# Performance work log

Hardware: AMD Instinct MI355X
Metric: run time of the kernel (lower is better)

Reference implementation:

```python
import jax, jax.numpy as jnp
import numpy as np

N_NODES = 50000
N_EDGES = 800000
D_IN = 256
D_HID = 256
D_OUT = 128


def setup_inputs() -> dict:
    key = jax.random.key(0)
    ks = jax.random.split(key, 6)
    z = jax.random.normal(ks[0], (N_NODES, D_IN), dtype=jnp.float32)
    edge_index = jax.random.randint(ks[1], (2, N_EDGES), 0, N_NODES, dtype=jnp.int32)
    W1 = jax.random.normal(ks[2], (D_IN, D_HID), dtype=jnp.float32) / np.sqrt(D_IN).astype(np.float32)
    b1 = jnp.zeros((D_HID,), dtype=jnp.float32)
    W2 = jax.random.normal(ks[3], (D_HID, D_OUT), dtype=jnp.float32) / np.sqrt(D_HID).astype(np.float32)
    b2 = jnp.zeros((D_OUT,), dtype=jnp.float32)
    return {"z": z, "edge_index": edge_index, "W1": W1, "b1": b1, "W2": W2, "b2": b2}


def _gcn_conv(x, W, b, src, dst, n_nodes):
    """GCNConv: x' = D^{-1/2} (A + I) D^{-1/2} (x W) + b (symmetric norm, self-loops)."""
    x = x @ W  # [n, d_out] dense transform first (as in PyG GCNConv)
    loop = jnp.arange(n_nodes, dtype=src.dtype)
    s = jnp.concatenate([src, loop])  # add self-loops
    d = jnp.concatenate([dst, loop])
    deg = jax.ops.segment_sum(jnp.ones(s.shape, dtype=x.dtype), d, num_segments=n_nodes)
    dinv = jnp.where(deg > 0, jax.lax.rsqrt(deg), 0.0)
    norm = dinv[s] * dinv[d]  # per-edge symmetric normalization
    msgs = x[s] * norm[:, None]  # gather + scale
    out = jax.ops.segment_sum(msgs, d, num_segments=n_nodes)  # scatter-add
    return out + b


def reference(z, edge_index, W1, b1, W2, b2):
    src, dst = edge_index[0], edge_index[1]
    n = z.shape[0]
    h = jax.nn.relu(_gcn_conv(z, W1, b1, src, dst, n))
    return _gcn_conv(h, W2, b2, src, dst, n)
```

## Files before the change

### kernel.cpp

```cpp
#include <hip/hip_runtime.h>


#define N_NODES 50000
#define N_EDGES 800000
#define D_IN    256
#define D_HID   256
#define D_OUT   128

typedef unsigned int uint32;
typedef unsigned short u16;

typedef __attribute__((ext_vector_type(8))) short bf16x8;
typedef __attribute__((ext_vector_type(4))) float f32x4;

__device__ __forceinline__ u16 f2bf_rne(float f) {
    union { float f; uint32 u; } c; c.f = f;
    uint32 u = c.u;
    u += 0x7FFFu + ((u >> 16) & 1u);
    return (u16)(u >> 16);
}
__device__ __forceinline__ float bf_lo(uint32 p) {
    union { uint32 u; float f; } c; c.u = p << 16; return c.f;
}
__device__ __forceinline__ float bf_hi(uint32 p) {
    union { uint32 u; float f; } c; c.u = p & 0xFFFF0000u; return c.f;
}


__global__ __launch_bounds__(256) void prep_kernel(const float* __restrict__ z,
                                                   const int* __restrict__ dst,
                                                   const float* __restrict__ W1,
                                                   const float* __restrict__ W2,
                                                   u16* __restrict__ zb,
                                                   u16* __restrict__ w1t,
                                                   u16* __restrict__ w2t,
                                                   int* __restrict__ cnt,
                                                   int* __restrict__ rank) {
    const int g = blockIdx.x * 256 + threadIdx.x;
    const int GT = gridDim.x * 256;

    for (int c = g; c < N_NODES * D_IN / 8; c += GT) {
        int i = c * 8;
        float4 a = *(const float4*)(z + i);
        float4 d = *(const float4*)(z + i + 4);
        uint4 pk;
        pk.x = (uint32)f2bf_rne(a.x) | ((uint32)f2bf_rne(a.y) << 16);
        pk.y = (uint32)f2bf_rne(a.z) | ((uint32)f2bf_rne(a.w) << 16);
        pk.z = (uint32)f2bf_rne(d.x) | ((uint32)f2bf_rne(d.y) << 16);
        pk.w = (uint32)f2bf_rne(d.z) | ((uint32)f2bf_rne(d.w) << 16);
        *(uint4*)(zb + i) = pk;
    }
    for (int idx = g; idx < D_IN * D_HID + D_HID * D_OUT; idx += GT) {
        if (idx < D_IN * D_HID) {
            int nrow = idx >> 8, kcol = idx & 255;
            w1t[idx] = f2bf_rne(W1[kcol * D_HID + nrow]);
        } else {
            int j = idx - D_IN * D_HID;
            int nrow = j >> 8, kcol = j & 255;
            w2t[j] = f2bf_rne(W2[kcol * D_OUT + nrow]);
        }
    }
    for (int i = g; i < N_EDGES; i += GT)
        rank[i] = atomicAdd(&cnt[dst[i]], 1);
}


__global__ __launch_bounds__(1024) void scan_kernel(const int* __restrict__ cnt,
                                                    float* __restrict__ dinv,
                                                    int* __restrict__ row_ptr, int n) {
    __shared__ int wtot[16];
    __shared__ int carry_s;
    const int t = threadIdx.x;
    const int lane = t & 63, w = t >> 6;
    if (t == 0) carry_s = 0;
    __syncthreads();

    const int n4 = n >> 2;
    for (int base = 0; base < n4; base += 1024) {
        int i4 = base + t;
        int4 v = make_int4(0, 0, 0, 0);
        if (i4 < n4) v = ((const int4*)cnt)[i4];
        int s = v.x + v.y + v.z + v.w;
        int x = s;
        #pragma unroll
        for (int off = 1; off < 64; off <<= 1) {
            int u = __shfl_up(x, off, 64);
            if (lane >= off) x += u;
        }
        if (lane == 63) wtot[w] = x;
        __syncthreads();

        int wbase = 0;
        #pragma unroll
        for (int j = 0; j < 16; ++j) if (j < w) wbase += wtot[j];
        int excl = carry_s + wbase + x - s;
        if (i4 < n4) {
            int4 rp;
            rp.x = excl;
            rp.y = rp.x + v.x;
            rp.z = rp.y + v.y;
            rp.w = rp.z + v.z;
            ((int4*)row_ptr)[i4] = rp;
            float4 dv;
            dv.x = rsqrtf((float)(v.x + 1));
            dv.y = rsqrtf((float)(v.y + 1));
            dv.z = rsqrtf((float)(v.z + 1));
            dv.w = rsqrtf((float)(v.w + 1));
            ((float4*)dinv)[i4] = dv;
        }
        __syncthreads();
        if (t == 0) {
            int tot = 0;
            #pragma unroll
            for (int j = 0; j < 16; ++j) tot += wtot[j];
            carry_s += tot;
        }
        __syncthreads();
    }
    if (t == 0) row_ptr[n] = carry_s;
}


__global__ void fill_kernel(const int* __restrict__ src, const int* __restrict__ dst,
                            const int* __restrict__ rank, const int* __restrict__ row_ptr,
                            int* __restrict__ col, int n_edges) {
    int i = blockIdx.x * blockDim.x + threadIdx.x;
    if (i < n_edges)
        col[row_ptr[dst[i]] + rank[i]] = src[i];
}


template <int NT>
__global__ __launch_bounds__(256, 4) void gemm_bf16_kernel(const u16* __restrict__ A,
                                                           const u16* __restrict__ BT,
                                                           u16* __restrict__ C, int M) {
    const int K = 256;
    __shared__ short As[128 * 32];
    __shared__ short Bs[128 * 32];

    const int m0 = blockIdx.x * 128;
    const int n0 = blockIdx.y * 128;
    const int t  = threadIdx.x;
    const int w  = t >> 6;
    const int lane = t & 63;
    const int lm = lane & 15;
    const int lq = lane >> 4;
    const int wm = w & 1;
    const int wn = w >> 1;

    f32x4 acc[4][4] = {};

    for (int k0 = 0; k0 < K; k0 += 32) {
        #pragma unroll
        for (int j = 0; j < 2; ++j) {
            int c = w * 128 + j * 64 + lane;
            int row = c >> 2;
            int kc = k0 + (c & 3) * 8;
            int gm = m0 + row; if (gm >= M) gm = M - 1;
            const u16* gpa = A  + (size_t)gm * K + kc;
            const u16* gpb = BT + (size_t)(n0 + row) * K + kc;
            __builtin_amdgcn_global_load_lds(
                (const __attribute__((address_space(1))) void*)gpa,
                (__attribute__((address_space(3))) void*)(As + (w * 128 + j * 64) * 8),
                16, 0, 0);
            __builtin_amdgcn_global_load_lds(
                (const __attribute__((address_space(1))) void*)gpb,
                (__attribute__((address_space(3))) void*)(Bs + (w * 128 + j * 64) * 8),
                16, 0, 0);
        }
        __syncthreads();

        bf16x8 af[4], bf[4];
        #pragma unroll
        for (int mt = 0; mt < 4; ++mt)
            af[mt] = *(const bf16x8*)&As[(wm * 64 + mt * 16 + lm) * 32 + lq * 8];
        #pragma unroll
        for (int nt = 0; nt < 4; ++nt)
            bf[nt] = *(const bf16x8*)&Bs[(wn * 64 + nt * 16 + lm) * 32 + lq * 8];

        #pragma unroll
        for (int mt = 0; mt < 4; ++mt)
            #pragma unroll
            for (int nt = 0; nt < 4; ++nt)
                acc[mt][nt] = __builtin_amdgcn_mfma_f32_16x16x32_bf16(
                    af[mt], bf[nt], acc[mt][nt], 0, 0, 0);

        __syncthreads();
    }

    #pragma unroll
    for (int mt = 0; mt < 4; ++mt) {
        #pragma unroll
        for (int r = 0; r < 4; ++r) {
            int gm = m0 + wm * 64 + mt * 16 + lq * 4 + r;
            if (gm < M) {
                #pragma unroll
                for (int nt = 0; nt < 4; ++nt) {
                    int gn = n0 + wn * 64 + nt * 16 + lm;
                    C[(size_t)gm * NT + gn] = f2bf_rne(acc[mt][nt][r]);
                }
            }
        }
    }
}


template <int D, bool RELU, bool OUTBF>
__global__ __launch_bounds__(256) void aggregate_kernel(const u16* __restrict__ x,
                                                        const int* __restrict__ row_ptr,
                                                        const int* __restrict__ col,
                                                        const float* __restrict__ dinv,
                                                        const float* __restrict__ bias,
                                                        void* __restrict__ outp, int n_nodes) {
    constexpr int VPL = D / 64;
    int node = (blockIdx.x * blockDim.x + threadIdx.x) >> 6;
    int lane = threadIdx.x & 63;
    if (node >= n_nodes) return;
    const int c0 = lane * VPL;

    float di = dinv[node];
    float acc[4][VPL] = {};

    {
        float w = di * di;
        const u16* xs = x + (size_t)node * D + c0;
        if constexpr (VPL == 4) {
            uint2 p = *(const uint2*)xs;
            acc[0][0] = bf_lo(p.x) * w;
            acc[0][1] = bf_hi(p.x) * w;
            acc[0][2] = bf_lo(p.y) * w;
            acc[0][3] = bf_hi(p.y) * w;
        } else {
            uint32 p = *(const uint32*)xs;
            acc[0][0] = bf_lo(p) * w;
            acc[0][1] = bf_hi(p) * w;
        }
    }

    int e0 = row_ptr[node], e1 = row_ptr[node + 1];
    int e = e0;
    for (; e + 4 <= e1; e += 4) {
        #pragma unroll
        for (int u = 0; u < 4; ++u) {
            int s  = col[e + u];
            float w = dinv[s] * di;
            const u16* xs = x + (size_t)s * D + c0;
            if constexpr (VPL == 4) {
                uint2 p = *(const uint2*)xs;
                acc[u][0] = fmaf(bf_lo(p.x), w, acc[u][0]);
                acc[u][1] = fmaf(bf_hi(p.x), w, acc[u][1]);
                acc[u][2] = fmaf(bf_lo(p.y), w, acc[u][2]);
                acc[u][3] = fmaf(bf_hi(p.y), w, acc[u][3]);
            } else {
                uint32 p = *(const uint32*)xs;
                acc[u][0] = fmaf(bf_lo(p), w, acc[u][0]);
                acc[u][1] = fmaf(bf_hi(p), w, acc[u][1]);
            }
        }
    }
    for (; e < e1; ++e) {
        int s  = col[e];
        float w = dinv[s] * di;
        const u16* xs = x + (size_t)s * D + c0;
        if constexpr (VPL == 4) {
            uint2 p = *(const uint2*)xs;
            acc[0][0] = fmaf(bf_lo(p.x), w, acc[0][0]);
            acc[0][1] = fmaf(bf_hi(p.x), w, acc[0][1]);
            acc[0][2] = fmaf(bf_lo(p.y), w, acc[0][2]);
            acc[0][3] = fmaf(bf_hi(p.y), w, acc[0][3]);
        } else {
            uint32 p = *(const uint32*)xs;
            acc[0][0] = fmaf(bf_lo(p), w, acc[0][0]);
            acc[0][1] = fmaf(bf_hi(p), w, acc[0][1]);
        }
    }

    float v[VPL];
    #pragma unroll
    for (int j = 0; j < VPL; ++j) {
        float s = acc[0][j] + acc[1][j] + acc[2][j] + acc[3][j] + bias[c0 + j];
        v[j] = RELU ? fmaxf(s, 0.0f) : s;
    }

    if constexpr (OUTBF) {
        u16* op = (u16*)outp + (size_t)node * D + c0;
        if constexpr (VPL == 4) {
            uint2 pk;
            pk.x = (uint32)f2bf_rne(v[0]) | ((uint32)f2bf_rne(v[1]) << 16);
            pk.y = (uint32)f2bf_rne(v[2]) | ((uint32)f2bf_rne(v[3]) << 16);
            *(uint2*)op = pk;
        } else {
            *(uint32*)op = (uint32)f2bf_rne(v[0]) | ((uint32)f2bf_rne(v[1]) << 16);
        }
    } else {
        float* op = (float*)outp + (size_t)node * D + c0;
        #pragma unroll
        for (int j = 0; j < VPL; ++j) op[j] = v[j];
    }
}


extern "C" void kernel_launch(void* const* d_in, const int* in_sizes, int n_in,
                              void* d_out, int out_size, void* d_ws, size_t ws_size,
                              hipStream_t stream) {
    const float* z  = (const float*)d_in[0];
    const int*   ei = (const int*)d_in[1];
    const float* W1 = (const float*)d_in[2];
    const float* b1 = (const float*)d_in[3];
    const float* W2 = (const float*)d_in[4];
    const float* b2 = (const float*)d_in[5];
    float* out = (float*)d_out;

    const int Nn = N_NODES, E = N_EDGES;
    const int* srcp = ei;
    const int* dstp = ei + E;

    char* ws = (char*)d_ws;
    size_t off = 0;
    auto alloc = [&](size_t bytes) -> char* {
        char* p = ws + off;
        off += (bytes + 511) & ~(size_t)511;
        return p;
    };
    u16*   zb     = (u16*)  alloc((size_t)Nn * D_IN * 2);
    u16*   w1t    = (u16*)  alloc((size_t)D_IN * D_HID * 2);
    u16*   w2t    = (u16*)  alloc((size_t)D_HID * D_OUT * 2);
    u16*   x1b    = (u16*)  alloc((size_t)Nn * D_HID * 2);
    u16*   hb     = (u16*)  alloc((size_t)Nn * D_HID * 2);
    u16*   h2b    = (u16*)  alloc((size_t)Nn * D_OUT * 2);
    int*   cnt    = (int*)  alloc((size_t)Nn * 4);
    float* dinv   = (float*)alloc((size_t)Nn * 4);
    int*   row_ptr= (int*)  alloc((size_t)(Nn + 1) * 4);
    int*   rank   = (int*)  alloc((size_t)E * 4);
    int*   col    = (int*)  alloc((size_t)E * 4);

    hipMemsetAsync(cnt, 0, (size_t)Nn * 4, stream);
    prep_kernel<<<1024, 256, 0, stream>>>(z, dstp, W1, W2, zb, w1t, w2t, cnt, rank);
    scan_kernel<<<1, 1024, 0, stream>>>(cnt, dinv, row_ptr, Nn);
    fill_kernel<<<(E + 255) / 256, 256, 0, stream>>>(srcp, dstp, rank, row_ptr, col, E);
    {
        dim3 grid((Nn + 127) / 128, D_HID / 128);
        gemm_bf16_kernel<D_HID><<<grid, 256, 0, stream>>>(zb, w1t, x1b, Nn);
    }
    {
        int blocks = (Nn + 3) / 4;
        aggregate_kernel<D_HID, true, true><<<blocks, 256, 0, stream>>>(x1b, row_ptr, col, dinv, b1, hb, Nn);
    }
    {
        dim3 grid((Nn + 127) / 128, D_OUT / 128);
        gemm_bf16_kernel<D_OUT><<<grid, 256, 0, stream>>>(hb, w2t, h2b, Nn);
    }
    {
        int blocks = (Nn + 3) / 4;
        aggregate_kernel<D_OUT, false, false><<<blocks, 256, 0, stream>>>(h2b, row_ptr, col, dinv, b2, out, Nn);
    }
}
```

Measured before the change: 292.6 us.

## Precompute edge weights in CSR and gather full 16-byte rows per lane group

The fill kernel now stores each CSR entry as an (src, weight) pair with the symmetric normalization precomputed, so aggregation no longer does a dependent dinv[s] lookup per edge. The aggregate kernel is restructured so each lane loads 16 bytes (8 bf16), and a wavefront processes several edges at once across lane groups before reducing with cross-lane shuffles. This targets latency-bound gathers and small per-lane loads. In exchange the edge array doubles in size and a shuffle reduction is added per node, and for D=256 only one edge is processed per group step.

```diff
diff --git a/kernel.cpp b/kernel.cpp
--- a/kernel.cpp
+++ b/kernel.cpp
@@ -123,10 +123,14 @@
 
 __global__ void fill_kernel(const int* __restrict__ src, const int* __restrict__ dst,
                             const int* __restrict__ rank, const int* __restrict__ row_ptr,
-                            int* __restrict__ col, int n_edges) {
+                            const float* __restrict__ dinv,
+                            int2* __restrict__ edata, int n_edges) {
     int i = blockIdx.x * blockDim.x + threadIdx.x;
-    if (i < n_edges)
-        col[row_ptr[dst[i]] + rank[i]] = src[i];
+    if (i < n_edges) {
+        int s = src[i], d = dst[i];
+        float w = dinv[s] * dinv[d];
+        edata[row_ptr[d] + rank[i]] = make_int2(s, __float_as_int(w));
+    }
 }
 
 
@@ -205,97 +209,102 @@
 }
 
 
+__device__ __forceinline__ void upd8(float* a, uint4 p, float w) {
+    a[0] = fmaf(bf_lo(p.x), w, a[0]);
+    a[1] = fmaf(bf_hi(p.x), w, a[1]);
+    a[2] = fmaf(bf_lo(p.y), w, a[2]);
+    a[3] = fmaf(bf_hi(p.y), w, a[3]);
+    a[4] = fmaf(bf_lo(p.z), w, a[4]);
+    a[5] = fmaf(bf_hi(p.z), w, a[5]);
+    a[6] = fmaf(bf_lo(p.w), w, a[6]);
+    a[7] = fmaf(bf_hi(p.w), w, a[7]);
+}
+
 template <int D, bool RELU, bool OUTBF>
 __global__ __launch_bounds__(256) void aggregate_kernel(const u16* __restrict__ x,
                                                         const int* __restrict__ row_ptr,
-                                                        const int* __restrict__ col,
+                                                        const int2* __restrict__ edata,
                                                         const float* __restrict__ dinv,
                                                         const float* __restrict__ bias,
                                                         void* __restrict__ outp, int n_nodes) {
-    constexpr int VPL = D / 64;
+    constexpr int LPR = D / 8;
+    constexpr int EPW = 64 / LPR;
+    constexpr int U   = 8 / EPW;
+
     int node = (blockIdx.x * blockDim.x + threadIdx.x) >> 6;
-    int lane = threadIdx.x & 63;
     if (node >= n_nodes) return;
-    const int c0 = lane * VPL;
-
-    float di = dinv[node];
-    float acc[4][VPL] = {};
-
-    {
-        float w = di * di;
-        const u16* xs = x + (size_t)node * D + c0;
-        if constexpr (VPL == 4) {
-            uint2 p = *(const uint2*)xs;
-            acc[0][0] = bf_lo(p.x) * w;
-            acc[0][1] = bf_hi(p.x) * w;
-            acc[0][2] = bf_lo(p.y) * w;
-            acc[0][3] = bf_hi(p.y) * w;
-        } else {
-            uint32 p = *(const uint32*)xs;
-            acc[0][0] = bf_lo(p) * w;
-            acc[0][1] = bf_hi(p) * w;
-        }
-    }
-
-    int e0 = row_ptr[node], e1 = row_ptr[node + 1];
+    const int lane = threadIdx.x & 63;
+    const int grp  = lane / LPR;
+    const int l    = lane % LPR;
+
+    float acc[U][8];
+    #pragma unroll
+    for (int u = 0; u < U; ++u)
+        #pragma unroll
+        for (int j = 0; j < 8; ++j) acc[u][j] = 0.0f;
+
+    if (grp == 0) {
+        float di = dinv[node];
+        uint4 p = *(const uint4*)(x + (size_t)node * D + l * 8);
+        upd8(acc[0], p, di * di);
+    }
+
+    const int e0 = row_ptr[node], e1 = row_ptr[node + 1];
     int e = e0;
-    for (; e + 4 <= e1; e += 4) {
-        #pragma unroll
-        for (int u = 0; u < 4; ++u) {
-            int s  = col[e + u];
-            float w = dinv[s] * di;
-            const u16* xs = x + (size_t)s * D + c0;
-            if constexpr (VPL == 4) {
-                uint2 p = *(const uint2*)xs;
-                acc[u][0] = fmaf(bf_lo(p.x), w, acc[u][0]);
-                acc[u][1] = fmaf(bf_hi(p.x), w, acc[u][1]);
-                acc[u][2] = fmaf(bf_lo(p.y), w, acc[u][2]);
-                acc[u][3] = fmaf(bf_hi(p.y), w, acc[u][3]);
-            } else {
-                uint32 p = *(const uint32*)xs;
-                acc[u][0] = fmaf(bf_lo(p), w, acc[u][0]);
-                acc[u][1] = fmaf(bf_hi(p), w, acc[u][1]);
-            }
-        }
-    }
-    for (; e < e1; ++e) {
-        int s  = col[e];
-        float w = dinv[s] * di;
-        const u16* xs = x + (size_t)s * D + c0;
-        if constexpr (VPL == 4) {
-            uint2 p = *(const uint2*)xs;
-            acc[0][0] = fmaf(bf_lo(p.x), w, acc[0][0]);
-            acc[0][1] = fmaf(bf_hi(p.x), w, acc[0][1]);
-            acc[0][2] = fmaf(bf_lo(p.y), w, acc[0][2]);
-            acc[0][3] = fmaf(bf_hi(p.y), w, acc[0][3]);
-        } else {
-            uint32 p = *(const uint32*)xs;
-            acc[0][0] = fmaf(bf_lo(p), w, acc[0][0]);
-            acc[0][1] = fmaf(bf_hi(p), w, acc[0][1]);
-        }
-    }
-
-    float v[VPL];
+    for (; e + U * EPW <= e1; e += U * EPW) {
+        int2 q[U];
+        #pragma unroll
+        for (int u = 0; u < U; ++u)
+            q[u] = edata[e + u * EPW + grp];
+        #pragma unroll
+        for (int u = 0; u < U; ++u) {
+            uint4 p = *(const uint4*)(x + (size_t)q[u].x * D + l * 8);
+            upd8(acc[u], p, __int_as_float(q[u].y));
+        }
+    }
+    for (; e < e1; e += EPW) {
+        int ee = e + grp;
+        int2 q = (ee < e1) ? edata[ee] : make_int2(node, 0);
+        uint4 p = *(const uint4*)(x + (size_t)q.x * D + l * 8);
+        upd8(acc[0], p, __int_as_float(q.y));
+    }
+
+    float v[8];
     #pragma unroll
-    for (int j = 0; j < VPL; ++j) {
-        float s = acc[0][j] + acc[1][j] + acc[2][j] + acc[3][j] + bias[c0 + j];
-        v[j] = RELU ? fmaxf(s, 0.0f) : s;
-    }
-
-    if constexpr (OUTBF) {
-        u16* op = (u16*)outp + (size_t)node * D + c0;
-        if constexpr (VPL == 4) {
-            uint2 pk;
+    for (int j = 0; j < 8; ++j) {
+        float s = acc[0][j];
+        #pragma unroll
+        for (int u = 1; u < U; ++u) s += acc[u][j];
+        v[j] = s;
+    }
+
+    #pragma unroll
+    for (int m = LPR; m < 64; m <<= 1)
+        #pragma unroll
+        for (int j = 0; j < 8; ++j)
+            v[j] += __shfl_xor(v[j], m, 64);
+
+    if (grp == 0) {
+        #pragma unroll
+        for (int j = 0; j < 8; ++j) {
+            float s = v[j] + bias[l * 8 + j];
+            v[j] = RELU ? fmaxf(s, 0.0f) : s;
+        }
+        if constexpr (OUTBF) {
+            u16* op = (u16*)outp + (size_t)node * D + l * 8;
+            uint4 pk;
             pk.x = (uint32)f2bf_rne(v[0]) | ((uint32)f2bf_rne(v[1]) << 16);
             pk.y = (uint32)f2bf_rne(v[2]) | ((uint32)f2bf_rne(v[3]) << 16);
-            *(uint2*)op = pk;
+            pk.z = (uint32)f2bf_rne(v[4]) | ((uint32)f2bf_rne(v[5]) << 16);
+            pk.w = (uint32)f2bf_rne(v[6]) | ((uint32)f2bf_rne(v[7]) << 16);
+            *(uint4*)op = pk;
         } else {
-            *(uint32*)op = (uint32)f2bf_rne(v[0]) | ((uint32)f2bf_rne(v[1]) << 16);
-        }
-    } else {
-        float* op = (float*)outp + (size_t)node * D + c0;
-        #pragma unroll
-        for (int j = 0; j < VPL; ++j) op[j] = v[j];
+            float* op = (float*)outp + (size_t)node * D + l * 8;
+            float4 a = make_float4(v[0], v[1], v[2], v[3]);
+            float4 b = make_float4(v[4], v[5], v[6], v[7]);
+            *(float4*)op = a;
+            *(float4*)(op + 4) = b;
+        }
     }
 }
 
@@ -332,19 +341,19 @@
     float* dinv   = (float*)alloc((size_t)Nn * 4);
     int*   row_ptr= (int*)  alloc((size_t)(Nn + 1) * 4);
     int*   rank   = (int*)  alloc((size_t)E * 4);
-    int*   col    = (int*)  alloc((size_t)E * 4);
+    int2*  edata  = (int2*) alloc((size_t)E * 8);
 
     hipMemsetAsync(cnt, 0, (size_t)Nn * 4, stream);
     prep_kernel<<<1024, 256, 0, stream>>>(z, dstp, W1, W2, zb, w1t, w2t, cnt, rank);
     scan_kernel<<<1, 1024, 0, stream>>>(cnt, dinv, row_ptr, Nn);
-    fill_kernel<<<(E + 255) / 256, 256, 0, stream>>>(srcp, dstp, rank, row_ptr, col, E);
+    fill_kernel<<<(E + 255) / 256, 256, 0, stream>>>(srcp, dstp, rank, row_ptr, dinv, edata, E);
     {
         dim3 grid((Nn + 127) / 128, D_HID / 128);
         gemm_bf16_kernel<D_HID><<<grid, 256, 0, stream>>>(zb, w1t, x1b, Nn);
     }
     {
         int blocks = (Nn + 3) / 4;
-        aggregate_kernel<D_HID, true, true><<<blocks, 256, 0, stream>>>(x1b, row_ptr, col, dinv, b1, hb, Nn);
+        aggregate_kernel<D_HID, true, true><<<blocks, 256, 0, stream>>>(x1b, row_ptr, edata, dinv, b1, hb, Nn);
     }
     {
         dim3 grid((Nn + 127) / 128, D_OUT / 128);
@@ -352,6 +361,6 @@
     }
     {
         int blocks = (Nn + 3) / 4;
-        aggregate_kernel<D_OUT, false, false><<<blocks, 256, 0, stream>>>(h2b, row_ptr, col, dinv, b2, out, Nn);
-    }
-}
+        aggregate_kernel<D_OUT, false, false><<<blocks, 256, 0, stream>>>(h2b, row_ptr, edata, dinv, b2, out, Nn);
+    }
+}
```

New measurement: 301.5 us. 3.0% more time.
